# Kernel tuning notes

Hardware: AMD Instinct MI355X
Metric: run time of the kernel (lower is better)

## Reference

```python
import jax, jax.numpy as jnp
import numpy as np

TEMP = 0.05
EPS = 1e-8  # torch CosineSimilarity eps


def setup_inputs() -> dict:
    key = jax.random.key(0)
    k1, k2 = jax.random.split(key)
    feature1 = jax.random.normal(k1, (4096, 768), dtype=jnp.float32)
    feature2 = jax.random.normal(k2, (4096, 768), dtype=jnp.float32)
    return {"feature1": feature1, "feature2": feature2}


def reference(feature1, feature2):
    # cosine similarity via L2-normalize + GEMM (same math as broadcast cos_sim)
    n1 = feature1 / jnp.maximum(jnp.linalg.norm(feature1, axis=-1, keepdims=True), EPS)
    n2 = feature2 / jnp.maximum(jnp.linalg.norm(feature2, axis=-1, keepdims=True), EPS)
    logits = jnp.einsum("id,jd->ij", n1, n2) / TEMP  # [N, N]
    # cross-entropy with labels = arange(N) -> mean of -log_softmax diagonal
    logp = jax.nn.log_softmax(logits, axis=-1)
    loss = -jnp.mean(jnp.diagonal(logp))
    return loss
```

## Files before the change

### kernel.cpp

```cpp
#include <hip/hip_runtime.h>
#include <hip/hip_bf16.h>

#define NROWS 4096
#define DIM   768
#define NKT   12

typedef __attribute__((ext_vector_type(8))) short short8;
typedef __attribute__((ext_vector_type(4))) float f32x4;

#define GAS(p) ((const __attribute__((address_space(1))) void*)(p))
#define SAS(p) ((__attribute__((address_space(3))) void*)(p))

__device__ __forceinline__ unsigned short f2bf(float x) {
    unsigned int u = __builtin_bit_cast(unsigned int, x);
    u += 0x7fffu + ((u >> 16) & 1u);
    return (unsigned short)(u >> 16);
}

__global__ __launch_bounds__(256) void k_norm(const float* __restrict__ f1,
                                              const float* __restrict__ f2,
                                              unsigned short* __restrict__ n1,
                                              unsigned short* __restrict__ n2,
                                              float* __restrict__ rowsum) {
    int b = blockIdx.x;
    int wid = threadIdx.x >> 6, lane = threadIdx.x & 63;
    int rowidx = b * 4 + wid;
    const float* src = (rowidx < NROWS) ? f1 : f2;
    unsigned short* dst = (rowidx < NROWS) ? n1 : n2;
    int row = rowidx & (NROWS - 1);
    const float4* srow = (const float4*)(src + (size_t)row * DIM);
    float4 v[3];
    float ss = 0.f;
#pragma unroll
    for (int r = 0; r < 3; ++r) {
        v[r] = srow[lane + 64 * r];
        ss += v[r].x * v[r].x + v[r].y * v[r].y + v[r].z * v[r].z + v[r].w * v[r].w;
    }
#pragma unroll
    for (int off = 32; off; off >>= 1) ss += __shfl_xor(ss, off);
    float inv = 1.0f / fmaxf(sqrtf(ss), 1e-8f);
    ushort4* drow = (ushort4*)(dst + (size_t)row * DIM);
#pragma unroll
    for (int r = 0; r < 3; ++r) {
        ushort4 o;
        o.x = f2bf(v[r].x * inv);
        o.y = f2bf(v[r].y * inv);
        o.z = f2bf(v[r].z * inv);
        o.w = f2bf(v[r].w * inv);
        drow[lane + 64 * r] = o;
    }
    if (b == 0) {
        float4 z = {0.f, 0.f, 0.f, 0.f};
#pragma unroll
        for (int i = 0; i < 4; ++i) ((float4*)rowsum)[threadIdx.x + 256 * i] = z;
    }
}


#define BARRIER __builtin_amdgcn_s_barrier()
#define WAIT_LGKM0 do { asm volatile("s_waitcnt lgkmcnt(0)" ::: "memory"); \
                        __builtin_amdgcn_sched_barrier(0); } while (0)
#define WAIT_VM4   do { asm volatile("s_waitcnt vmcnt(4)" ::: "memory"); \
                        __builtin_amdgcn_sched_barrier(0); } while (0)

__global__ __launch_bounds__(512, 2) void k_gemm_lse(const unsigned short* __restrict__ n1,
                                                     const unsigned short* __restrict__ n2,
                                                     float* __restrict__ rowsum,
                                                     float* __restrict__ diag) {
    __shared__ alignas(16) char ldsbuf[131072];
    char* ldsc = (char*)ldsbuf;

    int wg = blockIdx.x;
    int swz = (wg & 7) * 32 + (wg >> 3);
    int bi = swz >> 4;
    int bj = swz & 15;

    int tid = threadIdx.x;
    int wid = tid >> 6;
    int lane = tid & 63;
    int l15 = lane & 15, lk = lane >> 4;
    int wr = wid >> 2, wc = wid & 3;

    const unsigned short* abase = n1 + (size_t)bi * 256 * DIM;
    const unsigned short* bbase = n2 + (size_t)bj * 256 * DIM;

    const int stoff = (tid >> 3) * DIM + (((tid & 7) ^ ((tid >> 3) & 7)) * 8);

    const int swzl = (lane & 7) << 4;
    const int lko0 = l15 * 128 + ((lk * 16) ^ swzl);
    const int lko1 = l15 * 128 + (((64 + lk * 16)) ^ swzl);

    char* LA[2];
    char* LB[2];
    LA[0] = ldsc + (0 * 4 + wr) * 16384;
    LA[1] = ldsc + (1 * 4 + wr) * 16384;
    LB[0] = ldsc + (0 * 4 + 2 + (wc >> 1)) * 16384 + (wc & 1) * (64 * 128);
    LB[1] = ldsc + (1 * 4 + 2 + (wc >> 1)) * 16384 + (wc & 1) * (64 * 128);

#define STG(b, slot, base, half, kt) do { \
    const unsigned short* _s = (base) + ((half) * 128) * DIM + (kt) * 64 + stoff; \
    char* _d = ldsc + ((b) * 4 + (slot)) * 16384 + wid * 1024; \
    __builtin_amdgcn_global_load_lds(GAS(_s), SAS(_d), 16, 0, 0); \
    __builtin_amdgcn_global_load_lds(GAS(_s + 64 * DIM), SAS(_d + 8192), 16, 0, 0); \
} while (0)

#define LDA_(b, qm) do { _Pragma("unroll") for (int m = 0; m < 4; ++m) { \
    const char* _p = LA[b] + ((qm) * 64 + m * 16) * 128; \
    a[m][0] = *(const short8*)(_p + lko0); \
    a[m][1] = *(const short8*)(_p + lko1); } } while (0)

#define LDB_(b, qn, breg) do { _Pragma("unroll") for (int n = 0; n < 2; ++n) { \
    const char* _p = LB[b] + ((qn) * 2 + n) * 16 * 128; \
    breg[n][0] = *(const short8*)(_p + lko0); \
    breg[n][1] = *(const short8*)(_p + lko1); } } while (0)

#define MM_(qm, qn, breg) do { _Pragma("unroll") for (int m = 0; m < 4; ++m) \
    _Pragma("unroll") for (int n = 0; n < 2; ++n) { \
    f32x4* _c = &acc[(qm) * 4 + m][(qn) * 2 + n]; \
    *_c = __builtin_amdgcn_mfma_f32_16x16x32_bf16(a[m][0], breg[n][0], *_c, 0, 0, 0); \
    *_c = __builtin_amdgcn_mfma_f32_16x16x32_bf16(a[m][1], breg[n][1], *_c, 0, 0, 0); } } while (0)

    short8 a[4][2], b0[2][2], b1[2][2];
    f32x4 acc[8][4] = {};

    STG(0, 0, abase, 0, 0); STG(0, 1, abase, 1, 0);
    STG(0, 2, bbase, 0, 0); STG(0, 3, bbase, 1, 0);
    STG(1, 2, bbase, 0, 1); STG(1, 3, bbase, 1, 1);
    WAIT_VM4;
    BARRIER;

    for (int t = 0; t < NKT; t += 2) {
        int t1 = t + 1;
        int t2 = (t + 2 < NKT) ? t + 2 : t + 2 - NKT;
        int t3 = (t + 3 < NKT) ? t + 3 : t + 3 - NKT;
        LDA_(0, 0); LDB_(0, 0, b0);
        STG(1, 0, abase, 0, t1);
        BARRIER; WAIT_LGKM0;
        __builtin_amdgcn_s_setprio(1); MM_(0, 0, b0); __builtin_amdgcn_s_setprio(0);
        BARRIER;
        LDB_(0, 1, b1);
        STG(1, 1, abase, 1, t1);
        BARRIER; WAIT_LGKM0;
        __builtin_amdgcn_s_setprio(1); MM_(0, 1, b1); __builtin_amdgcn_s_setprio(0);
        BARRIER;
        LDA_(0, 1);
        STG(0, 2, bbase, 0, t2);
        BARRIER; WAIT_LGKM0;
        __builtin_amdgcn_s_setprio(1); MM_(1, 1, b1); __builtin_amdgcn_s_setprio(0);
        BARRIER;
        STG(0, 3, bbase, 1, t2);
        BARRIER;
        __builtin_amdgcn_s_setprio(1); MM_(1, 0, b0); __builtin_amdgcn_s_setprio(0);
        WAIT_VM4;
        BARRIER;
        LDA_(1, 0); LDB_(1, 0, b0);
        STG(0, 0, abase, 0, t2);
        BARRIER; WAIT_LGKM0;
        __builtin_amdgcn_s_setprio(1); MM_(0, 0, b0); __builtin_amdgcn_s_setprio(0);
        BARRIER;
        LDB_(1, 1, b1);
        STG(0, 1, abase, 1, t2);
        BARRIER; WAIT_LGKM0;
        __builtin_amdgcn_s_setprio(1); MM_(0, 1, b1); __builtin_amdgcn_s_setprio(0);
        BARRIER;
        LDA_(1, 1);
        STG(1, 2, bbase, 0, t3);
        BARRIER; WAIT_LGKM0;
        __builtin_amdgcn_s_setprio(1); MM_(1, 1, b1); __builtin_amdgcn_s_setprio(0);
        BARRIER;
        STG(1, 3, bbase, 1, t3);
        BARRIER;
        __builtin_amdgcn_s_setprio(1); MM_(1, 0, b0); __builtin_amdgcn_s_setprio(0);
        WAIT_VM4;
        BARRIER;
    }

    __syncthreads();

    const bool dblk = (bi == bj);
    const int rowb = bi * 256 + wr * 128;
    const int colb = bj * 256 + wc * 64;
#pragma unroll
    for (int mi = 0; mi < 8; ++mi) {
#pragma unroll
        for (int r = 0; r < 4; ++r) {
            float s = 0.f;
            int gi = rowb + mi * 16 + lk * 4 + r;
#pragma unroll
            for (int ni = 0; ni < 4; ++ni) {
                float v = acc[mi][ni][r] * 20.0f;
                s += __expf(v);
                if (dblk) {
                    int gj = colb + ni * 16 + l15;
                    if (gi == gj) diag[gi] = v;
                }
            }
#pragma unroll
            for (int off = 1; off < 16; off <<= 1) s += __shfl_xor(s, off);
            if (l15 == 0) atomicAdd(rowsum + gi, s);
        }
    }
}

__global__ __launch_bounds__(1024) void k_final(const float* __restrict__ rowsum,
                                                const float* __restrict__ diag,
                                                float* __restrict__ out) {
    int tid = threadIdx.x;
    float s = 0.f;
#pragma unroll
    for (int i = 0; i < 4; ++i) {
        int idx = tid + 1024 * i;
        s += logf(rowsum[idx]) - diag[idx];
    }
#pragma unroll
    for (int off = 32; off; off >>= 1) s += __shfl_xor(s, off);
    __shared__ float red[16];
    if ((tid & 63) == 0) red[tid >> 6] = s;
    __syncthreads();
    if (tid == 0) {
        float tot = 0.f;
#pragma unroll
        for (int i = 0; i < 16; ++i) tot += red[i];
        out[0] = tot * (1.0f / NROWS);
    }
}

extern "C" void kernel_launch(void* const* d_in, const int* in_sizes, int n_in,
                              void* d_out, int out_size, void* d_ws, size_t ws_size,
                              hipStream_t stream) {
    const float* f1 = (const float*)d_in[0];
    const float* f2 = (const float*)d_in[1];
    float* out = (float*)d_out;

    char* ws = (char*)d_ws;
    unsigned short* n1 = (unsigned short*)ws;
    unsigned short* n2 = n1 + (size_t)NROWS * DIM;
    float* rowsum = (float*)(ws + 2 * (size_t)NROWS * DIM * sizeof(unsigned short));
    float* diag = rowsum + NROWS;

    k_norm<<<2048, 256, 0, stream>>>(f1, f2, n1, n2, rowsum);
    k_gemm_lse<<<256, 512, 0, stream>>>(n1, n2, rowsum, diag);
    k_final<<<1, 1024, 0, stream>>>(rowsum, diag, out);
}
```

Before: 104.1 us.

## Fuse final reduction into GEMM via last-block counter and peel pipeline tail

Removes the separate final-reduction kernel launch. Each GEMM workgroup increments a global counter, and the last workgroup to finish computes the log-sum minus diagonal reduction and writes the loss. The main K loop is also restructured so its last iteration is peeled: the old wraparound prefetches of tiles 0/1 that were never used are dropped, and the epilogue skips the redundant global loads. This trades one kernel launch and some wasted memory traffic for an atomic counter and a serialized tail reduction in a single workgroup.

```diff
diff --git a/kernel.cpp b/kernel.cpp
--- a/kernel.cpp
+++ b/kernel.cpp
@@ -21,7 +21,8 @@
                                               const float* __restrict__ f2,
                                               unsigned short* __restrict__ n1,
                                               unsigned short* __restrict__ n2,
-                                              float* __restrict__ rowsum) {
+                                              float* __restrict__ rowsum,
+                                              unsigned int* __restrict__ cnt) {
     int b = blockIdx.x;
     int wid = threadIdx.x >> 6, lane = threadIdx.x & 63;
     int rowidx = b * 4 + wid;
@@ -53,6 +54,7 @@
         float4 z = {0.f, 0.f, 0.f, 0.f};
 #pragma unroll
         for (int i = 0; i < 4; ++i) ((float4*)rowsum)[threadIdx.x + 256 * i] = z;
+        if (threadIdx.x == 0) *cnt = 0u;
     }
 }
 
@@ -62,11 +64,17 @@
                         __builtin_amdgcn_sched_barrier(0); } while (0)
 #define WAIT_VM4   do { asm volatile("s_waitcnt vmcnt(4)" ::: "memory"); \
                         __builtin_amdgcn_sched_barrier(0); } while (0)
+#define WAIT_VM0   do { asm volatile("s_waitcnt vmcnt(0)" ::: "memory"); \
+                        __builtin_amdgcn_sched_barrier(0); } while (0)
+#define PRIO1 __builtin_amdgcn_s_setprio(1)
+#define PRIO0 __builtin_amdgcn_s_setprio(0)
 
 __global__ __launch_bounds__(512, 2) void k_gemm_lse(const unsigned short* __restrict__ n1,
                                                      const unsigned short* __restrict__ n2,
                                                      float* __restrict__ rowsum,
-                                                     float* __restrict__ diag) {
+                                                     float* __restrict__ diag,
+                                                     unsigned int* __restrict__ cnt,
+                                                     float* __restrict__ out) {
     __shared__ alignas(16) char ldsbuf[131072];
     char* ldsc = (char*)ldsbuf;
 
@@ -129,53 +137,83 @@
     WAIT_VM4;
     BARRIER;
 
-    for (int t = 0; t < NKT; t += 2) {
-        int t1 = t + 1;
-        int t2 = (t + 2 < NKT) ? t + 2 : t + 2 - NKT;
-        int t3 = (t + 3 < NKT) ? t + 3 : t + 3 - NKT;
+    for (int t = 0; t + 3 < NKT; t += 2) {
+        int t1 = t + 1, t2 = t + 2, t3 = t + 3;
         LDA_(0, 0); LDB_(0, 0, b0);
         STG(1, 0, abase, 0, t1);
         BARRIER; WAIT_LGKM0;
-        __builtin_amdgcn_s_setprio(1); MM_(0, 0, b0); __builtin_amdgcn_s_setprio(0);
+        PRIO1; MM_(0, 0, b0); PRIO0;
         BARRIER;
         LDB_(0, 1, b1);
         STG(1, 1, abase, 1, t1);
         BARRIER; WAIT_LGKM0;
-        __builtin_amdgcn_s_setprio(1); MM_(0, 1, b1); __builtin_amdgcn_s_setprio(0);
+        PRIO1; MM_(0, 1, b1); PRIO0;
         BARRIER;
         LDA_(0, 1);
         STG(0, 2, bbase, 0, t2);
         BARRIER; WAIT_LGKM0;
-        __builtin_amdgcn_s_setprio(1); MM_(1, 1, b1); __builtin_amdgcn_s_setprio(0);
+        PRIO1; MM_(1, 1, b1); PRIO0;
         BARRIER;
         STG(0, 3, bbase, 1, t2);
         BARRIER;
-        __builtin_amdgcn_s_setprio(1); MM_(1, 0, b0); __builtin_amdgcn_s_setprio(0);
+        PRIO1; MM_(1, 0, b0); PRIO0;
         WAIT_VM4;
         BARRIER;
         LDA_(1, 0); LDB_(1, 0, b0);
         STG(0, 0, abase, 0, t2);
         BARRIER; WAIT_LGKM0;
-        __builtin_amdgcn_s_setprio(1); MM_(0, 0, b0); __builtin_amdgcn_s_setprio(0);
+        PRIO1; MM_(0, 0, b0); PRIO0;
         BARRIER;
         LDB_(1, 1, b1);
         STG(0, 1, abase, 1, t2);
         BARRIER; WAIT_LGKM0;
-        __builtin_amdgcn_s_setprio(1); MM_(0, 1, b1); __builtin_amdgcn_s_setprio(0);
+        PRIO1; MM_(0, 1, b1); PRIO0;
         BARRIER;
         LDA_(1, 1);
         STG(1, 2, bbase, 0, t3);
         BARRIER; WAIT_LGKM0;
-        __builtin_amdgcn_s_setprio(1); MM_(1, 1, b1); __builtin_amdgcn_s_setprio(0);
+        PRIO1; MM_(1, 1, b1); PRIO0;
         BARRIER;
         STG(1, 3, bbase, 1, t3);
         BARRIER;
-        __builtin_amdgcn_s_setprio(1); MM_(1, 0, b0); __builtin_amdgcn_s_setprio(0);
+        PRIO1; MM_(1, 0, b0); PRIO0;
         WAIT_VM4;
         BARRIER;
     }
 
-    __syncthreads();
+    {
+        LDA_(0, 0); LDB_(0, 0, b0);
+        STG(1, 0, abase, 0, NKT - 1);
+        BARRIER; WAIT_LGKM0;
+        PRIO1; MM_(0, 0, b0); PRIO0;
+        BARRIER;
+        LDB_(0, 1, b1);
+        STG(1, 1, abase, 1, NKT - 1);
+        BARRIER; WAIT_LGKM0;
+        PRIO1; MM_(0, 1, b1); PRIO0;
+        BARRIER;
+        LDA_(0, 1);
+        BARRIER; WAIT_LGKM0;
+        PRIO1; MM_(1, 1, b1); PRIO0;
+        BARRIER;
+        PRIO1; MM_(1, 0, b0); PRIO0;
+        WAIT_VM0;
+        BARRIER;
+        LDA_(1, 0); LDB_(1, 0, b0);
+        BARRIER; WAIT_LGKM0;
+        PRIO1; MM_(0, 0, b0); PRIO0;
+        BARRIER;
+        LDB_(1, 1, b1);
+        BARRIER; WAIT_LGKM0;
+        PRIO1; MM_(0, 1, b1); PRIO0;
+        BARRIER;
+        LDA_(1, 1);
+        BARRIER; WAIT_LGKM0;
+        PRIO1; MM_(1, 1, b1); PRIO0;
+        BARRIER;
+        PRIO1; MM_(1, 0, b0); PRIO0;
+        BARRIER;
+    }
 
     const bool dblk = (bi == bj);
     const int rowb = bi * 256 + wr * 128;
@@ -200,28 +238,37 @@
             if (l15 == 0) atomicAdd(rowsum + gi, s);
         }
     }
-}
-
-__global__ __launch_bounds__(1024) void k_final(const float* __restrict__ rowsum,
-                                                const float* __restrict__ diag,
-                                                float* __restrict__ out) {
-    int tid = threadIdx.x;
-    float s = 0.f;
-#pragma unroll
-    for (int i = 0; i < 4; ++i) {
-        int idx = tid + 1024 * i;
-        s += logf(rowsum[idx]) - diag[idx];
-    }
-#pragma unroll
-    for (int off = 32; off; off >>= 1) s += __shfl_xor(s, off);
-    __shared__ float red[16];
-    if ((tid & 63) == 0) red[tid >> 6] = s;
+
+    __threadfence();
+    unsigned int* flag = (unsigned int*)ldsc;
+    if (tid == 0) {
+        unsigned int old = __hip_atomic_fetch_add(cnt, 1u, __ATOMIC_ACQ_REL,
+                                                  __HIP_MEMORY_SCOPE_AGENT);
+        *flag = (old == 255u) ? 1u : 0u;
+    }
     __syncthreads();
-    if (tid == 0) {
-        float tot = 0.f;
-#pragma unroll
-        for (int i = 0; i < 16; ++i) tot += red[i];
-        out[0] = tot * (1.0f / NROWS);
+    if (*flag) {
+        float s = 0.f;
+#pragma unroll
+        for (int k = 0; k < 8; ++k) {
+            int idx = tid + 512 * k;
+            float rs = __hip_atomic_load(rowsum + idx, __ATOMIC_RELAXED,
+                                         __HIP_MEMORY_SCOPE_AGENT);
+            float dg = __hip_atomic_load(diag + idx, __ATOMIC_RELAXED,
+                                         __HIP_MEMORY_SCOPE_AGENT);
+            s += logf(rs) - dg;
+        }
+#pragma unroll
+        for (int off = 32; off; off >>= 1) s += __shfl_xor(s, off);
+        float* red = (float*)(ldsc + 64);
+        if (lane == 0) red[wid] = s;
+        __syncthreads();
+        if (tid == 0) {
+            float tot = 0.f;
+#pragma unroll
+            for (int i = 0; i < 8; ++i) tot += red[i];
+            out[0] = tot * (1.0f / NROWS);
+        }
     }
 }
 
@@ -237,8 +284,8 @@
     unsigned short* n2 = n1 + (size_t)NROWS * DIM;
     float* rowsum = (float*)(ws + 2 * (size_t)NROWS * DIM * sizeof(unsigned short));
     float* diag = rowsum + NROWS;
-
-    k_norm<<<2048, 256, 0, stream>>>(f1, f2, n1, n2, rowsum);
-    k_gemm_lse<<<256, 512, 0, stream>>>(n1, n2, rowsum, diag);
-    k_final<<<1, 1024, 0, stream>>>(rowsum, diag, out);
-}
+    unsigned int* cnt = (unsigned int*)(diag + NROWS);
+
+    k_norm<<<2048, 256, 0, stream>>>(f1, f2, n1, n2, rowsum, cnt);
+    k_gemm_lse<<<256, 512, 0, stream>>>(n1, n2, rowsum, diag, cnt, out);
+}
```

Result: slower. 131.5 us (+26.3%).

## Double-buffer A fragments and overlap LDS reads with MFMA phases

Applied to the files above, without the earlier changes.

Splits the A-operand register fragment into two buffers (aA/aB) so the LDS reads for the next quadrant are issued before the current MFMA block instead of after a barrier. The first quadrant's loads are hoisted before the loop and the last phase prefetches the next iteration's first fragments, software-pipelining LDS reads against matrix-core work. This raises register pressure under the 512x2 launch bound and makes the barrier and waitcnt ordering more delicate, since LDS reads now sit just before barriers that guard buffer reuse.

```diff
diff --git a/kernel.cpp b/kernel.cpp
--- a/kernel.cpp
+++ b/kernel.cpp
@@ -62,6 +62,8 @@
                         __builtin_amdgcn_sched_barrier(0); } while (0)
 #define WAIT_VM4   do { asm volatile("s_waitcnt vmcnt(4)" ::: "memory"); \
                         __builtin_amdgcn_sched_barrier(0); } while (0)
+#define PRIO1 __builtin_amdgcn_s_setprio(1)
+#define PRIO0 __builtin_amdgcn_s_setprio(0)
 
 __global__ __launch_bounds__(512, 2) void k_gemm_lse(const unsigned short* __restrict__ n1,
                                                      const unsigned short* __restrict__ n2,
@@ -104,23 +106,23 @@
     __builtin_amdgcn_global_load_lds(GAS(_s + 64 * DIM), SAS(_d + 8192), 16, 0, 0); \
 } while (0)
 
-#define LDA_(b, qm) do { _Pragma("unroll") for (int m = 0; m < 4; ++m) { \
+#define LDA_(b, qm, areg) do { _Pragma("unroll") for (int m = 0; m < 4; ++m) { \
     const char* _p = LA[b] + ((qm) * 64 + m * 16) * 128; \
-    a[m][0] = *(const short8*)(_p + lko0); \
-    a[m][1] = *(const short8*)(_p + lko1); } } while (0)
+    areg[m][0] = *(const short8*)(_p + lko0); \
+    areg[m][1] = *(const short8*)(_p + lko1); } } while (0)
 
 #define LDB_(b, qn, breg) do { _Pragma("unroll") for (int n = 0; n < 2; ++n) { \
     const char* _p = LB[b] + ((qn) * 2 + n) * 16 * 128; \
     breg[n][0] = *(const short8*)(_p + lko0); \
     breg[n][1] = *(const short8*)(_p + lko1); } } while (0)
 
-#define MM_(qm, qn, breg) do { _Pragma("unroll") for (int m = 0; m < 4; ++m) \
+#define MM_(qm, qn, areg, breg) do { _Pragma("unroll") for (int m = 0; m < 4; ++m) \
     _Pragma("unroll") for (int n = 0; n < 2; ++n) { \
     f32x4* _c = &acc[(qm) * 4 + m][(qn) * 2 + n]; \
-    *_c = __builtin_amdgcn_mfma_f32_16x16x32_bf16(a[m][0], breg[n][0], *_c, 0, 0, 0); \
-    *_c = __builtin_amdgcn_mfma_f32_16x16x32_bf16(a[m][1], breg[n][1], *_c, 0, 0, 0); } } while (0)
-
-    short8 a[4][2], b0[2][2], b1[2][2];
+    *_c = __builtin_amdgcn_mfma_f32_16x16x32_bf16(areg[m][0], breg[n][0], *_c, 0, 0, 0); \
+    *_c = __builtin_amdgcn_mfma_f32_16x16x32_bf16(areg[m][1], breg[n][1], *_c, 0, 0, 0); } } while (0)
+
+    short8 aA[4][2], aB[4][2], b0[2][2], b1[2][2];
     f32x4 acc[8][4] = {};
 
     STG(0, 0, abase, 0, 0); STG(0, 1, abase, 1, 0);
@@ -128,50 +130,51 @@
     STG(1, 2, bbase, 0, 1); STG(1, 3, bbase, 1, 1);
     WAIT_VM4;
     BARRIER;
+    LDA_(0, 0, aA); LDB_(0, 0, b0);
 
     for (int t = 0; t < NKT; t += 2) {
         int t1 = t + 1;
         int t2 = (t + 2 < NKT) ? t + 2 : t + 2 - NKT;
         int t3 = (t + 3 < NKT) ? t + 3 : t + 3 - NKT;
-        LDA_(0, 0); LDB_(0, 0, b0);
         STG(1, 0, abase, 0, t1);
         BARRIER; WAIT_LGKM0;
-        __builtin_amdgcn_s_setprio(1); MM_(0, 0, b0); __builtin_amdgcn_s_setprio(0);
-        BARRIER;
         LDB_(0, 1, b1);
+        PRIO1; MM_(0, 0, aA, b0); PRIO0;
+        BARRIER;
         STG(1, 1, abase, 1, t1);
         BARRIER; WAIT_LGKM0;
-        __builtin_amdgcn_s_setprio(1); MM_(0, 1, b1); __builtin_amdgcn_s_setprio(0);
-        BARRIER;
-        LDA_(0, 1);
+        LDA_(0, 1, aB);
+        PRIO1; MM_(0, 1, aA, b1); PRIO0;
+        BARRIER;
         STG(0, 2, bbase, 0, t2);
         BARRIER; WAIT_LGKM0;
-        __builtin_amdgcn_s_setprio(1); MM_(1, 1, b1); __builtin_amdgcn_s_setprio(0);
+        PRIO1; MM_(1, 1, aB, b1); PRIO0;
         BARRIER;
         STG(0, 3, bbase, 1, t2);
         BARRIER;
-        __builtin_amdgcn_s_setprio(1); MM_(1, 0, b0); __builtin_amdgcn_s_setprio(0);
+        PRIO1; MM_(1, 0, aB, b0); PRIO0;
         WAIT_VM4;
-        BARRIER;
-        LDA_(1, 0); LDB_(1, 0, b0);
+        LDA_(1, 0, aA); LDB_(1, 0, b0);
+        BARRIER;
         STG(0, 0, abase, 0, t2);
         BARRIER; WAIT_LGKM0;
-        __builtin_amdgcn_s_setprio(1); MM_(0, 0, b0); __builtin_amdgcn_s_setprio(0);
-        BARRIER;
         LDB_(1, 1, b1);
+        PRIO1; MM_(0, 0, aA, b0); PRIO0;
+        BARRIER;
         STG(0, 1, abase, 1, t2);
         BARRIER; WAIT_LGKM0;
-        __builtin_amdgcn_s_setprio(1); MM_(0, 1, b1); __builtin_amdgcn_s_setprio(0);
-        BARRIER;
-        LDA_(1, 1);
+        LDA_(1, 1, aB);
+        PRIO1; MM_(0, 1, aA, b1); PRIO0;
+        BARRIER;
         STG(1, 2, bbase, 0, t3);
         BARRIER; WAIT_LGKM0;
-        __builtin_amdgcn_s_setprio(1); MM_(1, 1, b1); __builtin_amdgcn_s_setprio(0);
+        PRIO1; MM_(1, 1, aB, b1); PRIO0;
         BARRIER;
         STG(1, 3, bbase, 1, t3);
         BARRIER;
-        __builtin_amdgcn_s_setprio(1); MM_(1, 0, b0); __builtin_amdgcn_s_setprio(0);
+        PRIO1; MM_(1, 0, aB, b0); PRIO0;
         WAIT_VM4;
+        LDA_(0, 0, aA); LDB_(0, 0, b0);
         BARRIER;
     }
 
```

Result: slower. 106.3 us (+2.1%).
